# Kernel tuning notes

Hardware: AMD Instinct MI355X
Metric: run time of the kernel (lower is better)

Reference implementation:

```python
import jax, jax.numpy as jnp
import numpy as np

# Config (matches init_kwargs)
B, L, D = 2, 2048, 1024
QH, KVH, HD, FFN = 8, 2, 128, 4096
EPS = 1.1920929e-07  # torch RMSNorm default eps = finfo(float32).eps


def _rope_ts():
    d2 = HD // 2
    freq_exp = (2.0 / HD) * jnp.arange(d2, dtype=jnp.float32)
    return 10000.0 ** freq_exp  # [d2]


def _rope(x):
    # x: [B, L, H, HD], rotated in fp32 (matches x.float() in source)
    d2 = HD // 2
    pos = jnp.arange(L, dtype=jnp.float32)
    rad = pos[:, None] / _rope_ts()[None, :]          # [L, d2]
    s = jnp.sin(rad)[None, :, None, :]                # [1, L, 1, d2]
    c = jnp.cos(rad)[None, :, None, :]
    xf = x.astype(jnp.float32)
    x1, x2 = xf[..., :d2], xf[..., d2:]
    return jnp.concatenate([x1 * c - x2 * s, x2 * c + x1 * s], axis=-1).astype(x.dtype)


def _rmsnorm(x, w):
    xf = x.astype(jnp.float32)
    r = jax.lax.rsqrt(jnp.mean(xf * xf, axis=-1, keepdims=True) + EPS)
    return (xf * r).astype(x.dtype) * w


def setup_inputs() -> dict:
    key = jax.random.key(0)
    ks = jax.random.split(key, 9)
    s = 0.02
    return {
        "x": jax.random.normal(ks[0], (B, L, D), dtype=jnp.float32),
        "ln1_w": jnp.ones((D,), dtype=jnp.float32),
        "wq": jax.random.normal(ks[1], (D, QH * HD), dtype=jnp.float32) * s,
        "wk": jax.random.normal(ks[2], (D, KVH * HD), dtype=jnp.float32) * s,
        "wv": jax.random.normal(ks[3], (D, KVH * HD), dtype=jnp.float32) * s,
        "wo": jax.random.normal(ks[4], (QH * HD, D), dtype=jnp.float32) * s,
        "ln2_w": jnp.ones((D,), dtype=jnp.float32),
        "wg": jax.random.normal(ks[5], (D, FFN), dtype=jnp.float32) * s,
        "wu": jax.random.normal(ks[6], (D, FFN), dtype=jnp.float32) * s,
        "wd": jax.random.normal(ks[7], (FFN, D), dtype=jnp.float32) * s,
    }


def reference(x, ln1_w, wq, wk, wv, wo, ln2_w, wg, wu, wd):
    residual = x
    h = _rmsnorm(x, ln1_w)

    q = _rope((h @ wq).reshape(B, L, QH, HD))          # [B,L,QH,HD]
    k = _rope((h @ wk).reshape(B, L, KVH, HD))         # [B,L,KVH,HD]
    v = (h @ wv).reshape(B, L, KVH, HD)

    rep = QH // KVH  # kv_map = floor(arange(QH)*KVH/QH) == repeat each kv head `rep` times
    qh = jnp.transpose(q, (0, 2, 1, 3)).astype(jnp.float32)                       # [B,QH,L,HD]
    kh = jnp.transpose(jnp.repeat(k, rep, axis=2), (0, 2, 1, 3)).astype(jnp.float32)
    vh = jnp.transpose(jnp.repeat(v, rep, axis=2), (0, 2, 1, 3)).astype(jnp.float32)

    scores = jnp.einsum("bhqd,bhkd->bhqk", qh, kh) / jnp.sqrt(jnp.float32(HD))    # [B,QH,L,L]
    causal = jnp.triu(jnp.ones((L, L), dtype=bool), 1)
    scores = jnp.where(causal, -jnp.inf, scores)
    attn = jax.nn.softmax(scores, axis=-1)
    ctx = jnp.einsum("bhqk,bhkd->bhqd", attn, vh)                                 # [B,QH,L,HD]
    ctx = jnp.transpose(ctx, (0, 2, 1, 3)).reshape(B, L, QH * HD).astype(x.dtype)

    x = ctx @ wo + residual
    residual = x
    h = _rmsnorm(x, ln2_w)
    return (jax.nn.silu(h @ wg) * (h @ wu)) @ wd + residual
```

## Files before the change

### kernel.cpp

```cpp
#include <hip/hip_runtime.h>
#include <hip/hip_bf16.h>
#include <math.h>

#define B_ 2
#define L_ 2048
#define D_ 1024
#define QH_ 8
#define KVH_ 2
#define HD_ 128
#define FFN_ 4096
#define T_ (B_ * L_)
#define EPS_ 1.1920929e-07f

typedef __bf16 bf16x8 __attribute__((ext_vector_type(8)));
typedef float floatx4 __attribute__((ext_vector_type(4)));
typedef unsigned short ushortx8 __attribute__((ext_vector_type(8)));
typedef unsigned short ushortx4 __attribute__((ext_vector_type(4)));

__device__ __forceinline__ unsigned short f2bf(float f) {
  union { float f; unsigned int u; } v;
  v.f = f;
  unsigned int r = v.u + 0x7FFFu + ((v.u >> 16) & 1u);
  return (unsigned short)(r >> 16);
}
__device__ __forceinline__ float bf2f(unsigned short u) {
  union { unsigned int u; float f; } v;
  v.u = ((unsigned int)u) << 16;
  return v.f;
}
__device__ __forceinline__ void gload_lds16(const void* g, void* l) {
  __builtin_amdgcn_global_load_lds((const __attribute__((address_space(1))) void*)g,
                                   (__attribute__((address_space(3))) void*)l, 16, 0, 0);
}

__device__ __forceinline__ void strip_tc(const float* __restrict__ in,
                                         unsigned short* __restrict__ out,
                                         int K, int N, int n0, int k0) {
  __shared__ float tile[4][32][33];
  int t = threadIdx.x;
  int tx = t & 31, ty = t >> 5;
#pragma unroll
  for (int s = 0; s < 4; s++)
#pragma unroll
    for (int r0 = 0; r0 < 4; r0++) {
      int r = ty + r0 * 8;
      tile[s][r][tx] = in[(size_t)(k0 + s * 32 + r) * N + n0 + tx];
    }
  __syncthreads();
  int nr = t >> 3, kq = t & 7;
#pragma unroll
  for (int s = 0; s < 4; s++) {
    ushortx4 o4;
#pragma unroll
    for (int j = 0; j < 4; j++) o4[j] = f2bf(tile[s][kq * 4 + j][nr]);
    *(ushortx4*)(out + (size_t)(n0 + nr) * K + k0 + s * 32 + kq * 4) = o4;
  }
}

__device__ __forceinline__ void rmsnorm_row(const float* __restrict__ x,
                                            const float* __restrict__ w,
                                            unsigned short* __restrict__ o, int row) {
  __shared__ float red[4];
  int t = threadIdx.x;
  const float* xr = x + (size_t)row * D_;
  float4 xv = *(const float4*)(xr + t * 4);
  float ss = xv.x * xv.x + xv.y * xv.y + xv.z * xv.z + xv.w * xv.w;
#pragma unroll
  for (int off = 32; off >= 1; off >>= 1) ss += __shfl_xor(ss, off);
  if ((t & 63) == 0) red[t >> 6] = ss;
  __syncthreads();
  float total = red[0] + red[1] + red[2] + red[3];
  float r = rsqrtf(total * (1.0f / (float)D_) + EPS_);
  float4 wv = *(const float4*)(w + t * 4);
  unsigned short* op = o + (size_t)row * D_ + t * 4;
  op[0] = f2bf(xv.x * r * wv.x);
  op[1] = f2bf(xv.y * r * wv.y);
  op[2] = f2bf(xv.z * r * wv.z);
  op[3] = f2bf(xv.w * r * wv.w);
}

__global__ __launch_bounds__(256) void prep_all(
    const float* __restrict__ wq, const float* __restrict__ wk,
    const float* __restrict__ wv, const float* __restrict__ wo,
    const float* __restrict__ wg, const float* __restrict__ wu,
    const float* __restrict__ wd, unsigned short* __restrict__ wT,
    const float* __restrict__ x, const float* __restrict__ ln1w,
    unsigned short* __restrict__ h_bf) {
  int bid = blockIdx.x;
  if (bid < 3712) {
    const float* in;
    unsigned short* out;
    int K, N, nt, base;
    if (bid < 256)       { in = wq; out = wT;            K = 1024; N = 1024; nt = 32;  base = 0; }
    else if (bid < 320)  { in = wk; out = wT + 1048576;  K = 1024; N = 256;  nt = 8;   base = 256; }
    else if (bid < 384)  { in = wv; out = wT + 1310720;  K = 1024; N = 256;  nt = 8;   base = 320; }
    else if (bid < 640)  { in = wo; out = wT + 1572864;  K = 1024; N = 1024; nt = 32;  base = 384; }
    else if (bid < 1664) { in = wg; out = wT + 2621440;  K = 1024; N = 4096; nt = 128; base = 640; }
    else if (bid < 2688) { in = wu; out = wT + 6815744;  K = 1024; N = 4096; nt = 128; base = 1664; }
    else                 { in = wd; out = wT + 11010048; K = 4096; N = 1024; nt = 32;  base = 2688; }
    int idx = bid - base;
    strip_tc(in, out, K, N, (idx % nt) * 32, (idx / nt) * 128);
  } else {
    rmsnorm_row(x, ln1w, h_bf, bid - 3712);
  }
}

__global__ __launch_bounds__(256) void rmsnorm_bf16_kernel(const float* __restrict__ x,
                                                           const float* __restrict__ w,
                                                           unsigned short* __restrict__ o) {
  rmsnorm_row(x, w, o, blockIdx.x);
}

template <int EPI, int KH>
__global__ __launch_bounds__(256, 3) void gemm_bf16(const unsigned short* __restrict__ A,
                                                    const unsigned short* __restrict__ BT,
                                                    const float* __restrict__ R,
                                                    float* __restrict__ C,
                                                    int M, int N, int K) {
  __shared__ unsigned short As[KH][64 * 32];
  __shared__ unsigned short Bs[KH][128 * 32];
  int t = threadIdx.x;
  int lane = t & 63, wave = t >> 6;
  int m0 = blockIdx.y * 64, n0 = blockIdx.x * 128;

  int row_a = t >> 2;
  int kc = ((t & 3) ^ ((t >> 3) & 3)) * 8;
  const unsigned short* ga0 = A + (size_t)(m0 + row_a) * K + kc;
  const unsigned short* gb0 = BT + (size_t)(n0 + row_a) * K + kc;
  const unsigned short* gb1 = BT + (size_t)(n0 + 64 + row_a) * K + kc;

  int wm = (wave & 1) * 32, wn = (wave >> 1) * 64;
  int fr = lane & 15, quad = lane >> 4;
  int sw = (quad ^ ((fr >> 1) & 3)) * 8;

  floatx4 acc[2][4];
#pragma unroll
  for (int i = 0; i < 2; i++)
#pragma unroll
    for (int j = 0; j < 4; j++) acc[i][j] = (floatx4){0.f, 0.f, 0.f, 0.f};

  for (int k0 = 0; k0 < K; k0 += 32 * KH) {
#pragma unroll
    for (int h = 0; h < KH; h++) {
      int ko = k0 + h * 32;
      gload_lds16(ga0 + ko, As[h] + wave * 512);
      gload_lds16(gb0 + ko, Bs[h] + wave * 512);
      gload_lds16(gb1 + ko, Bs[h] + 2048 + wave * 512);
    }
    __syncthreads();
#pragma unroll
    for (int h = 0; h < KH; h++) {
      const unsigned short* arp = As[h] + (size_t)(wm + fr) * 32 + sw;
      const unsigned short* brp = Bs[h] + (size_t)(wn + fr) * 32 + sw;
      bf16x8 af[2], bfr[4];
#pragma unroll
      for (int i = 0; i < 2; i++)
        af[i] = __builtin_bit_cast(bf16x8, *(const ushortx8*)(arp + i * 16 * 32));
#pragma unroll
      for (int j = 0; j < 4; j++)
        bfr[j] = __builtin_bit_cast(bf16x8, *(const ushortx8*)(brp + j * 16 * 32));
#pragma unroll
      for (int i = 0; i < 2; i++)
#pragma unroll
        for (int j = 0; j < 4; j++)
          acc[i][j] = __builtin_amdgcn_mfma_f32_16x16x32_bf16(af[i], bfr[j], acc[i][j], 0, 0, 0);
    }
    __syncthreads();
  }

  int orow = m0 + wm + quad * 4;
  int ocol = n0 + wn + fr;
#pragma unroll
  for (int i = 0; i < 2; i++) {
#pragma unroll
    for (int r = 0; r < 4; r++) {
      int row = orow + i * 16 + r;
#pragma unroll
      for (int j = 0; j < 4; j++) {
        size_t idx = (size_t)row * N + ocol + j * 16;
        float v = acc[i][j][r];
        if (EPI == 1) C[idx] = v + R[idx];
        else C[idx] = v + C[idx];
      }
    }
  }
}

__global__ __launch_bounds__(256) void gemm_qkv(const unsigned short* __restrict__ A,
                                                const unsigned short* __restrict__ BT,
                                                unsigned short* __restrict__ qb,
                                                unsigned short* __restrict__ Kb,
                                                unsigned short* __restrict__ Vt) {
  constexpr int K = 1024;
  __shared__ unsigned short smem[24576];
  int t = threadIdx.x;
  int lane = t & 63, wave = t >> 6;
  int bx = blockIdx.x;
  int m0 = blockIdx.y * 64, n0 = bx * 128;

  int row_a = t >> 2;
  int kc = ((t & 3) ^ ((t >> 3) & 3)) * 8;
  const unsigned short* ga0 = A + (size_t)(m0 + row_a) * K + kc;
  const unsigned short* gb0 = BT + (size_t)(n0 + row_a) * K + kc;
  const unsigned short* gb1 = BT + (size_t)(n0 + 64 + row_a) * K + kc;

  int wm = (wave & 1) * 32, wn = (wave >> 1) * 64;
  int fr = lane & 15, quad = lane >> 4;
  int sw = (quad ^ ((fr >> 1) & 3)) * 8;

  floatx4 acc[2][4];
#pragma unroll
  for (int i = 0; i < 2; i++)
#pragma unroll
    for (int j = 0; j < 4; j++) acc[i][j] = (floatx4){0.f, 0.f, 0.f, 0.f};

  for (int k0 = 0; k0 < K; k0 += 128) {
#pragma unroll
    for (int h = 0; h < 4; h++) {
      int ko = k0 + h * 32;
      gload_lds16(ga0 + ko, smem + h * 2048 + wave * 512);
      gload_lds16(gb0 + ko, smem + 8192 + h * 4096 + wave * 512);
      gload_lds16(gb1 + ko, smem + 8192 + h * 4096 + 2048 + wave * 512);
    }
    __syncthreads();
#pragma unroll
    for (int h = 0; h < 4; h++) {
      const unsigned short* arp = smem + h * 2048 + (size_t)(wm + fr) * 32 + sw;
      const unsigned short* brp = smem + 8192 + h * 4096 + (size_t)(wn + fr) * 32 + sw;
      bf16x8 af[2], bfr[4];
#pragma unroll
      for (int i = 0; i < 2; i++)
        af[i] = __builtin_bit_cast(bf16x8, *(const ushortx8*)(arp + i * 16 * 32));
#pragma unroll
      for (int j = 0; j < 4; j++)
        bfr[j] = __builtin_bit_cast(bf16x8, *(const ushortx8*)(brp + j * 16 * 32));
#pragma unroll
      for (int i = 0; i < 2; i++)
#pragma unroll
        for (int j = 0; j < 4; j++)
          acc[i][j] = __builtin_amdgcn_mfma_f32_16x16x32_bf16(af[i], bfr[j], acc[i][j], 0, 0, 0);
    }
    __syncthreads();
  }

  unsigned short* scr = smem;
#pragma unroll
  for (int i = 0; i < 2; i++)
#pragma unroll
    for (int r = 0; r < 4; r++)
#pragma unroll
      for (int j = 0; j < 4; j++)
        scr[(size_t)(wm + quad * 4 + i * 16 + r) * 136 + wn + fr + j * 16] =
            f2bf(acc[i][j][r]);
  __syncthreads();

  if (bx < 10) {
    int row = t >> 2, dq = (t & 3) * 16;
    int tok = m0 + row, pos = tok & (L_ - 1), b = tok >> 11;
    float scale_ = (bx < 8) ? 0.08838834764831843f : 1.0f;
    unsigned short lo[16], hi[16];
#pragma unroll
    for (int m = 0; m < 16; m++) {
      int d2 = dq + m;
      float x1 = bf2f(scr[(size_t)row * 136 + d2]);
      float x2 = bf2f(scr[(size_t)row * 136 + d2 + 64]);
      float inv_ts = expf(-0.14391156831f * (float)d2);
      float rad = (float)pos * inv_ts;
      float s = sinf(rad), c = cosf(rad);
      lo[m] = f2bf((x1 * c - x2 * s) * scale_);
      hi[m] = f2bf((x2 * c + x1 * s) * scale_);
    }
    if (bx < 8) {
      unsigned short* dst = qb + (size_t)tok * 1024 + bx * 128;
      *(ushortx8*)(dst + dq) = *(const ushortx8*)(lo);
      *(ushortx8*)(dst + dq + 8) = *(const ushortx8*)(lo + 8);
      *(ushortx8*)(dst + 64 + dq) = *(const ushortx8*)(hi);
      *(ushortx8*)(dst + 64 + dq + 8) = *(const ushortx8*)(hi + 8);
    } else {
      int kvh = bx - 8, bk = b * KVH_ + kvh, swk = pos & 15;
      unsigned short* dst = Kb + ((size_t)bk * L_ + pos) * HD_;
      int c0 = dq >> 3;
      *(ushortx8*)(dst + ((c0) ^ swk) * 8) = *(const ushortx8*)(lo);
      *(ushortx8*)(dst + ((c0 + 1) ^ swk) * 8) = *(const ushortx8*)(lo + 8);
      *(ushortx8*)(dst + ((c0 + 8) ^ swk) * 8) = *(const ushortx8*)(hi);
      *(ushortx8*)(dst + ((c0 + 9) ^ swk) * 8) = *(const ushortx8*)(hi + 8);
    }
  } else {
    int kvh = bx - 10;
    int b = m0 >> 11, key0 = m0 & (L_ - 1), bk = b * KVH_ + kvh;
    int hd = t >> 1, half = t & 1;
#pragma unroll
    for (int c = 0; c < 4; c++) {
      int cp = half * 4 + c, kcc = cp ^ (hd & 7);
      ushortx8 ob;
#pragma unroll
      for (int j = 0; j < 8; j++) ob[j] = scr[(size_t)(kcc * 8 + j) * 136 + hd];
      *(ushortx8*)(Vt + ((size_t)bk * HD_ + hd) * L_ + key0 + cp * 8) = ob;
    }
  }
}

__global__ __launch_bounds__(256, 3) void gemm_gateup(const unsigned short* __restrict__ A,
                                                      const unsigned short* __restrict__ BgT,
                                                      const unsigned short* __restrict__ BuT,
                                                      unsigned short* __restrict__ Cb,
                                                      int M, int K) {
  constexpr int N = FFN_;
  __shared__ unsigned short As[2][128 * 32];
  __shared__ unsigned short Bgs[2][64 * 32];
  __shared__ unsigned short Bus[2][64 * 32];
  int t = threadIdx.x;
  int lane = t & 63, wave = t >> 6;
  int m0 = blockIdx.y * 128, n0 = blockIdx.x * 64;

  int row_a = t >> 2;
  int kc = ((t & 3) ^ ((t >> 3) & 3)) * 8;
  const unsigned short* ga0 = A + (size_t)(m0 + row_a) * K + kc;
  const unsigned short* ga1 = A + (size_t)(m0 + 64 + row_a) * K + kc;
  const unsigned short* gg0 = BgT + (size_t)(n0 + row_a) * K + kc;
  const unsigned short* gu0 = BuT + (size_t)(n0 + row_a) * K + kc;

  int wm = wave * 32;
  int fr = lane & 15, quad = lane >> 4;
  int sw = (quad ^ ((fr >> 1) & 3)) * 8;

  floatx4 accg[2][4], accu[2][4];
#pragma unroll
  for (int i = 0; i < 2; i++)
#pragma unroll
    for (int j = 0; j < 4; j++) {
      accg[i][j] = (floatx4){0.f, 0.f, 0.f, 0.f};
      accu[i][j] = (floatx4){0.f, 0.f, 0.f, 0.f};
    }

  for (int k0 = 0; k0 < K; k0 += 64) {
#pragma unroll
    for (int h = 0; h < 2; h++) {
      int ko = k0 + h * 32;
      gload_lds16(ga0 + ko, As[h] + wave * 512);
      gload_lds16(ga1 + ko, As[h] + 2048 + wave * 512);
      gload_lds16(gg0 + ko, Bgs[h] + wave * 512);
      gload_lds16(gu0 + ko, Bus[h] + wave * 512);
    }
    __syncthreads();
#pragma unroll
    for (int h = 0; h < 2; h++) {
      const unsigned short* arp = As[h] + (size_t)(wm + fr) * 32 + sw;
      const unsigned short* grp = Bgs[h] + (size_t)fr * 32 + sw;
      const unsigned short* urp = Bus[h] + (size_t)fr * 32 + sw;
      bf16x8 af[2], bg[4], bu[4];
#pragma unroll
      for (int i = 0; i < 2; i++)
        af[i] = __builtin_bit_cast(bf16x8, *(const ushortx8*)(arp + i * 16 * 32));
#pragma unroll
      for (int j = 0; j < 4; j++) {
        bg[j] = __builtin_bit_cast(bf16x8, *(const ushortx8*)(grp + j * 16 * 32));
        bu[j] = __builtin_bit_cast(bf16x8, *(const ushortx8*)(urp + j * 16 * 32));
      }
#pragma unroll
      for (int i = 0; i < 2; i++)
#pragma unroll
        for (int j = 0; j < 4; j++) {
          accg[i][j] = __builtin_amdgcn_mfma_f32_16x16x32_bf16(af[i], bg[j], accg[i][j], 0, 0, 0);
          accu[i][j] = __builtin_amdgcn_mfma_f32_16x16x32_bf16(af[i], bu[j], accu[i][j], 0, 0, 0);
        }
    }
    __syncthreads();
  }

  int orow = m0 + wm + quad * 4;
  int ocol = n0 + fr;
#pragma unroll
  for (int i = 0; i < 2; i++) {
#pragma unroll
    for (int r = 0; r < 4; r++) {
      int row = orow + i * 16 + r;
#pragma unroll
      for (int j = 0; j < 4; j++) {
        float g = accg[i][j][r];
        float u = accu[i][j][r];
        Cb[(size_t)row * N + ocol + j * 16] = f2bf(g / (1.f + __expf(-g)) * u);
      }
    }
  }
}

__global__ __launch_bounds__(256) void attn_mfma(const unsigned short* __restrict__ qb,
                                                 const unsigned short* __restrict__ Kb,
                                                 const unsigned short* __restrict__ Vt,
                                                 unsigned short* __restrict__ ctx) {
  __shared__ unsigned short Ks[64 * 128];
  __shared__ unsigned short Vs[128 * 64];
  __shared__ unsigned short Ps[4][16 * 72];
  int id = blockIdx.x;
  int bh = id & 15;
  int p_ = id >> 4;
  int qt = (p_ < 16) ? p_ : 47 - p_;
  int b = bh >> 3, h = bh & 7;
  int bk = b * KVH_ + (h >> 2);
  int q0 = qt * 64;
  int t = threadIdx.x, lane = t & 63, w = t >> 6;
  int fr = lane & 15, quad = lane >> 4;

  int pos = q0 + w * 16 + fr;
  const unsigned short* qrow = qb + (size_t)(b * L_ + pos) * 1024 + h * HD_;
  bf16x8 qf[4];
#pragma unroll
  for (int kb = 0; kb < 4; kb++)
    qf[kb] = __builtin_bit_cast(bf16x8, *(const ushortx8*)(qrow + kb * 32 + quad * 8));

  floatx4 o_acc[8];
#pragma unroll
  for (int nt = 0; nt < 8; nt++) o_acc[nt] = (floatx4){0.f, 0.f, 0.f, 0.f};
  float l_r[4] = {0.f, 0.f, 0.f, 0.f};
  unsigned short* Psw = Ps[w];
  const unsigned short* kgb = Kb + (size_t)bk * L_ * HD_;
  const unsigned short* vgb = Vt + (size_t)bk * HD_ * L_;
  int rowg0 = q0 + w * 16 + quad * 4;

  for (int kt = 0; kt <= qt; kt++) {
    int kstart = kt * 64;
    bool diag = (kt == qt);
    __syncthreads();
    const unsigned short* ksrc = kgb + (size_t)kstart * HD_;
#pragma unroll
    for (int it = 0; it < 4; it++) {
      int sl = it * 4 + w;
      gload_lds16(ksrc + sl * 512 + lane * 8, Ks + sl * 512);
    }
#pragma unroll
    for (int it = 0; it < 4; it++) {
      int sl = it * 4 + w;
      gload_lds16(vgb + (size_t)(sl * 8 + (lane >> 3)) * L_ + kstart + (lane & 7) * 8,
                  Vs + sl * 512);
    }
    __syncthreads();

    floatx4 s_acc[4];
#pragma unroll
    for (int jt = 0; jt < 4; jt++) s_acc[jt] = (floatx4){0.f, 0.f, 0.f, 0.f};
#pragma unroll
    for (int kb = 0; kb < 4; kb++) {
#pragma unroll
      for (int jt = 0; jt < 4; jt++) {
        bf16x8 kf = __builtin_bit_cast(
            bf16x8, *(const ushortx8*)(Ks + (jt * 16 + fr) * 128 +
                                       (((kb * 4 + quad) ^ fr) * 8)));
        s_acc[jt] = __builtin_amdgcn_mfma_f32_16x16x32_bf16(qf[kb], kf, s_acc[jt], 0, 0, 0);
      }
    }

#pragma unroll
    for (int jt = 0; jt < 4; jt++) {
#pragma unroll
      for (int r = 0; r < 4; r++) {
        float pp;
        if (diag) {
          int keyg = kstart + jt * 16 + fr;
          pp = (keyg <= rowg0 + r) ? __expf(s_acc[jt][r]) : 0.f;
        } else {
          pp = __expf(s_acc[jt][r]);
        }
        l_r[r] += pp;
        Psw[(quad * 4 + r) * 72 + jt * 16 + fr] = f2bf(pp);
      }
    }
    bf16x8 pf0 = __builtin_bit_cast(bf16x8, *(const ushortx8*)(Psw + fr * 72 + quad * 8));
    bf16x8 pf1 =
        __builtin_bit_cast(bf16x8, *(const ushortx8*)(Psw + fr * 72 + 32 + quad * 8));
#pragma unroll
    for (int nt = 0; nt < 8; nt++) {
      bf16x8 vf0 = __builtin_bit_cast(
          bf16x8,
          *(const ushortx8*)(Vs + (nt * 16 + fr) * 64 + ((quad ^ (fr & 7)) * 8)));
      bf16x8 vf1 = __builtin_bit_cast(
          bf16x8,
          *(const ushortx8*)(Vs + (nt * 16 + fr) * 64 + (((4 + quad) ^ (fr & 7)) * 8)));
      o_acc[nt] = __builtin_amdgcn_mfma_f32_16x16x32_bf16(pf0, vf0, o_acc[nt], 0, 0, 0);
      o_acc[nt] = __builtin_amdgcn_mfma_f32_16x16x32_bf16(pf1, vf1, o_acc[nt], 0, 0, 0);
    }
  }

#pragma unroll
  for (int r = 0; r < 4; r++) {
    l_r[r] += __shfl_xor(l_r[r], 1);
    l_r[r] += __shfl_xor(l_r[r], 2);
    l_r[r] += __shfl_xor(l_r[r], 4);
    l_r[r] += __shfl_xor(l_r[r], 8);
  }

  unsigned short* ob =
      ctx + (size_t)(b * L_ + q0 + w * 16 + quad * 4) * 1024 + h * HD_ + fr;
#pragma unroll
  for (int r = 0; r < 4; r++) {
    float inv = 1.f / l_r[r];
    unsigned short* orow = ob + (size_t)r * 1024;
#pragma unroll
    for (int nt = 0; nt < 8; nt++) orow[nt * 16] = f2bf(o_acc[nt][r] * inv);
  }
}

extern "C" void kernel_launch(void* const* d_in, const int* in_sizes, int n_in,
                              void* d_out, int out_size, void* d_ws, size_t ws_size,
                              hipStream_t stream) {
  const float* x    = (const float*)d_in[0];
  const float* ln1w = (const float*)d_in[1];
  const float* wq   = (const float*)d_in[2];
  const float* wk   = (const float*)d_in[3];
  const float* wvp  = (const float*)d_in[4];
  const float* wo   = (const float*)d_in[5];
  const float* ln2w = (const float*)d_in[6];
  const float* wg   = (const float*)d_in[7];
  const float* wu   = (const float*)d_in[8];
  const float* wd   = (const float*)d_in[9];
  float* out = (float*)d_out;
  char* ws = (char*)d_ws;

  unsigned short* wT = (unsigned short*)ws;
  unsigned short* wqkvT = wT;
  unsigned short* woT = wT + 1572864;
  unsigned short* wgT = wT + 2621440;
  unsigned short* wuT = wT + 6815744;
  unsigned short* wdT = wT + 11010048;
  unsigned short* h_bf = (unsigned short*)(ws + 30408704);
  unsigned short* qb = (unsigned short*)(ws + 38797312);
  unsigned short* h2_bf = (unsigned short*)(ws + 51380224);
  unsigned short* Kb = (unsigned short*)(ws + 59768832);
  unsigned short* Vt = (unsigned short*)(ws + 61865984);
  unsigned short* gu = (unsigned short*)(ws + 59768832);
  unsigned short* ctx_bf = h_bf;

  dim3 blk(256);

  prep_all<<<3712 + T_, blk, 0, stream>>>(wq, wk, wvp, wo, wg, wu, wd, wT, x, ln1w, h_bf);
  gemm_qkv<<<dim3(12, 64), blk, 0, stream>>>(h_bf, wqkvT, qb, Kb, Vt);
  attn_mfma<<<512, blk, 0, stream>>>(qb, Kb, Vt, ctx_bf);
  gemm_bf16<1, 4><<<dim3(8, 64), blk, 0, stream>>>(ctx_bf, woT, x, out, T_, 1024, 1024);
  rmsnorm_bf16_kernel<<<T_, blk, 0, stream>>>(out, ln2w, h2_bf);
  gemm_gateup<<<dim3(64, 32), blk, 0, stream>>>(h2_bf, wgT, wuT, gu, T_, 1024);
  gemm_bf16<2, 4><<<dim3(8, 64), blk, 0, stream>>>(gu, wdT, nullptr, out, T_, 1024, FFN_);
}
```

Measured before the change: 369.8 us.

## Rewrite gate/up GEMM with 256x256 tiles, 8 waves, 4-stage async pipeline

Replaces the gate/up fused GEMM with a 512-thread kernel that computes a 256-row by 128-column output tile. The B tile interleaves gate and up weight rows in 16-row groups, so one fragment path feeds both. K tiles go through a 4-deep ring of LDS buffers using async global-to-LDS loads. Fine-grained vmcnt waits and a single barrier per K step replace the previous load-then-sync pattern, and s_setprio is raised around the MFMA bursts. The aim is to hide load latency and raise operand reuse per LDS read, at the cost of 128KB of LDS per block and higher register pressure, which limits occupancy.

Result: slower. 380.1 us (+2.8%).

```diff
diff --git a/kernel.cpp b/kernel.cpp
--- a/kernel.cpp
+++ b/kernel.cpp
@@ -300,86 +300,108 @@
   }
 }
 
-__global__ __launch_bounds__(256, 3) void gemm_gateup(const unsigned short* __restrict__ A,
-                                                      const unsigned short* __restrict__ BgT,
-                                                      const unsigned short* __restrict__ BuT,
-                                                      unsigned short* __restrict__ Cb,
-                                                      int M, int K) {
-  constexpr int N = FFN_;
-  __shared__ unsigned short As[2][128 * 32];
-  __shared__ unsigned short Bgs[2][64 * 32];
-  __shared__ unsigned short Bus[2][64 * 32];
+__global__ __launch_bounds__(512, 2) void gemm_gateup8(
+    const unsigned short* __restrict__ A,
+    const unsigned short* __restrict__ BgT,
+    const unsigned short* __restrict__ BuT,
+    unsigned short* __restrict__ Cb) {
+  constexpr int K = 1024;
+  constexpr int NTILES = K / 32;
+  __shared__ unsigned short As[4][256 * 32];
+  __shared__ unsigned short Bs[4][256 * 32];
+
   int t = threadIdx.x;
   int lane = t & 63, wave = t >> 6;
-  int m0 = blockIdx.y * 128, n0 = blockIdx.x * 64;
+  int m0 = blockIdx.y * 256;
+  int n0l = blockIdx.x * 128;
 
   int row_a = t >> 2;
   int kc = ((t & 3) ^ ((t >> 3) & 3)) * 8;
   const unsigned short* ga0 = A + (size_t)(m0 + row_a) * K + kc;
-  const unsigned short* ga1 = A + (size_t)(m0 + 64 + row_a) * K + kc;
-  const unsigned short* gg0 = BgT + (size_t)(n0 + row_a) * K + kc;
-  const unsigned short* gu0 = BuT + (size_t)(n0 + row_a) * K + kc;
-
-  int wm = wave * 32;
+  const unsigned short* ga1 = ga0 + (size_t)128 * K;
+  int rb0 = row_a, rb1 = row_a + 128;
+  const unsigned short* gb0 =
+      ((rb0 & 31) < 16 ? BgT : BuT) +
+      (size_t)(n0l + (rb0 >> 5) * 16 + (rb0 & 15)) * K + kc;
+  const unsigned short* gb1 =
+      ((rb1 & 31) < 16 ? BgT : BuT) +
+      (size_t)(n0l + (rb1 >> 5) * 16 + (rb1 & 15)) * K + kc;
+
+  int wm = wave >> 2;
+  int wn = wave & 3;
   int fr = lane & 15, quad = lane >> 4;
   int sw = (quad ^ ((fr >> 1) & 3)) * 8;
 
-  floatx4 accg[2][4], accu[2][4];
-#pragma unroll
-  for (int i = 0; i < 2; i++)
-#pragma unroll
-    for (int j = 0; j < 4; j++) {
-      accg[i][j] = (floatx4){0.f, 0.f, 0.f, 0.f};
-      accu[i][j] = (floatx4){0.f, 0.f, 0.f, 0.f};
-    }
-
-  for (int k0 = 0; k0 < K; k0 += 64) {
-#pragma unroll
-    for (int h = 0; h < 2; h++) {
-      int ko = k0 + h * 32;
-      gload_lds16(ga0 + ko, As[h] + wave * 512);
-      gload_lds16(ga1 + ko, As[h] + 2048 + wave * 512);
-      gload_lds16(gg0 + ko, Bgs[h] + wave * 512);
-      gload_lds16(gu0 + ko, Bus[h] + wave * 512);
-    }
-    __syncthreads();
-#pragma unroll
-    for (int h = 0; h < 2; h++) {
-      const unsigned short* arp = As[h] + (size_t)(wm + fr) * 32 + sw;
-      const unsigned short* grp = Bgs[h] + (size_t)fr * 32 + sw;
-      const unsigned short* urp = Bus[h] + (size_t)fr * 32 + sw;
-      bf16x8 af[2], bg[4], bu[4];
-#pragma unroll
-      for (int i = 0; i < 2; i++)
-        af[i] = __builtin_bit_cast(bf16x8, *(const ushortx8*)(arp + i * 16 * 32));
-#pragma unroll
-      for (int j = 0; j < 4; j++) {
-        bg[j] = __builtin_bit_cast(bf16x8, *(const ushortx8*)(grp + j * 16 * 32));
-        bu[j] = __builtin_bit_cast(bf16x8, *(const ushortx8*)(urp + j * 16 * 32));
-      }
-#pragma unroll
-      for (int i = 0; i < 2; i++)
-#pragma unroll
-        for (int j = 0; j < 4; j++) {
-          accg[i][j] = __builtin_amdgcn_mfma_f32_16x16x32_bf16(af[i], bg[j], accg[i][j], 0, 0, 0);
-          accu[i][j] = __builtin_amdgcn_mfma_f32_16x16x32_bf16(af[i], bu[j], accu[i][j], 0, 0, 0);
-        }
-    }
-    __syncthreads();
-  }
-
-  int orow = m0 + wm + quad * 4;
-  int ocol = n0 + fr;
-#pragma unroll
-  for (int i = 0; i < 2; i++) {
+  floatx4 acc[8][4];
+#pragma unroll
+  for (int i = 0; i < 8; i++)
+#pragma unroll
+    for (int j = 0; j < 4; j++) acc[i][j] = (floatx4){0.f, 0.f, 0.f, 0.f};
+
+#define GU_STAGE(kt_)                                              \
+  {                                                                \
+    int ko_ = (kt_) * 32;                                          \
+    unsigned short* as_ = (unsigned short*)As[(kt_) & 3];          \
+    unsigned short* bs_ = (unsigned short*)Bs[(kt_) & 3];          \
+    gload_lds16(ga0 + ko_, as_ + wave * 512);                      \
+    gload_lds16(ga1 + ko_, as_ + 4096 + wave * 512);               \
+    gload_lds16(gb0 + ko_, bs_ + wave * 512);                      \
+    gload_lds16(gb1 + ko_, bs_ + 4096 + wave * 512);               \
+  }
+
+#define GU_COMPUTE(kt_)                                                        \
+  {                                                                            \
+    const unsigned short* asr = As[(kt_) & 3];                                 \
+    const unsigned short* bsr = Bs[(kt_) & 3];                                 \
+    bf16x8 bfr[4], af[8];                                                      \
+    _Pragma("unroll") for (int j = 0; j < 4; j++) bfr[j] =                     \
+        __builtin_bit_cast(bf16x8,                                             \
+            *(const ushortx8*)(bsr + (size_t)(wn * 64 + j * 16 + fr) * 32 + sw)); \
+    _Pragma("unroll") for (int i = 0; i < 8; i++) af[i] =                      \
+        __builtin_bit_cast(bf16x8,                                             \
+            *(const ushortx8*)(asr + (size_t)(wm * 128 + i * 16 + fr) * 32 + sw)); \
+    __builtin_amdgcn_s_setprio(1);                                             \
+    _Pragma("unroll") for (int i = 0; i < 8; i++)                              \
+        _Pragma("unroll") for (int j = 0; j < 4; j++) acc[i][j] =              \
+            __builtin_amdgcn_mfma_f32_16x16x32_bf16(af[i], bfr[j], acc[i][j],  \
+                                                    0, 0, 0);                  \
+    __builtin_amdgcn_s_setprio(0);                                             \
+  }
+
+  GU_STAGE(0);
+  GU_STAGE(1);
+  GU_STAGE(2);
+
+  for (int kt = 0; kt < NTILES - 2; kt++) {
+    asm volatile("s_waitcnt vmcnt(8)" ::: "memory");
+    __builtin_amdgcn_s_barrier();
+    asm volatile("" ::: "memory");
+    if (kt < NTILES - 3) GU_STAGE(kt + 3);
+    GU_COMPUTE(kt);
+  }
+  asm volatile("s_waitcnt vmcnt(4)" ::: "memory");
+  __builtin_amdgcn_s_barrier();
+  asm volatile("" ::: "memory");
+  GU_COMPUTE(NTILES - 2);
+  asm volatile("s_waitcnt vmcnt(0)" ::: "memory");
+  __builtin_amdgcn_s_barrier();
+  asm volatile("" ::: "memory");
+  GU_COMPUTE(NTILES - 1);
+
+#undef GU_STAGE
+#undef GU_COMPUTE
+
+#pragma unroll
+  for (int i = 0; i < 8; i++) {
+    int row = m0 + wm * 128 + i * 16 + quad * 4;
 #pragma unroll
     for (int r = 0; r < 4; r++) {
-      int row = orow + i * 16 + r;
-#pragma unroll
-      for (int j = 0; j < 4; j++) {
-        float g = accg[i][j][r];
-        float u = accu[i][j][r];
-        Cb[(size_t)row * N + ocol + j * 16] = f2bf(g / (1.f + __expf(-g)) * u);
+#pragma unroll
+      for (int jj = 0; jj < 2; jj++) {
+        float g = acc[i][2 * jj][r];
+        float u = acc[i][2 * jj + 1][r];
+        int colL = n0l + (wn * 2 + jj) * 16 + fr;
+        Cb[(size_t)(row + r) * FFN_ + colL] = f2bf(g / (1.f + __expf(-g)) * u);
       }
     }
   }
@@ -537,6 +559,6 @@
   attn_mfma<<<512, blk, 0, stream>>>(qb, Kb, Vt, ctx_bf);
   gemm_bf16<1, 4><<<dim3(8, 64), blk, 0, stream>>>(ctx_bf, woT, x, out, T_, 1024, 1024);
   rmsnorm_bf16_kernel<<<T_, blk, 0, stream>>>(out, ln2w, h2_bf);
-  gemm_gateup<<<dim3(64, 32), blk, 0, stream>>>(h2_bf, wgT, wuT, gu, T_, 1024);
+  gemm_gateup8<<<dim3(32, 16), dim3(512), 0, stream>>>(h2_bf, wgT, wuT, gu);
   gemm_bf16<2, 4><<<dim3(8, 64), blk, 0, stream>>>(gu, wdT, nullptr, out, T_, 1024, FFN_);
 }
```
